# Kernel tuning notes

Measured on AMD Instinct MI355X. Metric: run time of the kernel, lower is better.

Reference implementation:

```python
import jax, jax.numpy as jnp
import numpy as np

L, HID, H, D = 2, 128, 8, 16  # layers, hidden, heads, head_dim
N, E = 50000, 800000
CLAMP = 5.0
BN_SCALE = 1.0 / np.sqrt(1.0 + 1e-5)  # eval BN with running mean 0, var 1


def signed_sqrt(s):
    # sqrt(relu(s)) - sqrt(relu(-s)), with safe gradients at 0
    pos = jnp.sqrt(jnp.where(s > 0, s, 1.0))
    neg = jnp.sqrt(jnp.where(s < 0, -s, 1.0))
    return jnp.where(s > 0, pos, 0.0) - jnp.where(s < 0, neg, 0.0)


def setup_inputs() -> dict:
    key = jax.random.key(0)
    ks = jax.random.split(key, 32)
    sc = 0.05
    inp = {
        "x": jax.random.normal(ks[0], (N, HID), jnp.float32),
        "edge_index": jax.random.randint(ks[1], (2, E), 0, N, jnp.int64)
        if jax.config.jax_enable_x64 else jax.random.randint(ks[1], (2, E), 0, N, jnp.int32),
        "edge_attr": jax.random.normal(ks[2], (E, HID), jnp.float32),
        "Wq": jax.random.normal(ks[3], (L, HID, HID), jnp.float32) * sc,
        "bq": jnp.zeros((L, HID), jnp.float32),
        "Wk": jax.random.normal(ks[4], (L, HID, HID), jnp.float32) * sc,
        "Wv": jax.random.normal(ks[5], (L, HID, HID), jnp.float32) * sc,
        "We": jax.random.normal(ks[6], (L, HID, 2 * HID), jnp.float32) * sc,
        "be": jnp.zeros((L, 2 * HID), jnp.float32),
        "Aw": jax.random.normal(ks[7], (L, D, H, 1), jnp.float32) * 0.2,
        "VeRow": jax.random.normal(ks[8], (L, D, H, D), jnp.float32) * sc,
        "Woh": jax.random.normal(ks[9], (L, HID, HID), jnp.float32) * sc,
        "boh": jnp.zeros((L, HID), jnp.float32),
        "Woe": jax.random.normal(ks[10], (L, HID, HID), jnp.float32) * sc,
        "boe": jnp.zeros((L, HID), jnp.float32),
        "deg_coef": jax.random.normal(ks[11], (L, 1, HID, 2), jnp.float32) * 0.2,
        "W1": jax.random.normal(ks[12], (L, HID, 2 * HID), jnp.float32) * sc,
        "b1": jnp.zeros((L, 2 * HID), jnp.float32),
        "W2": jax.random.normal(ks[13], (L, 2 * HID, HID), jnp.float32) * sc,
        "b2": jnp.zeros((L, HID), jnp.float32),
    }
    return inp


def _forward(x, edge_attr, edge_index, Wq, bq, Wk, Wv, We, be, Aw, VeRow,
             Woh, boh, Woe, boe, deg_coef, W1, b1, W2, b2):
    src, dst = edge_index[0], edge_index[1]
    n = x.shape[0]
    deg = jax.ops.segment_sum(jnp.ones_like(dst, jnp.float32), dst, num_segments=n)
    log_deg = jnp.log(deg + 1.0)[:, None]  # [N,1]

    for l in range(L):
        Qh = (x @ Wq[l] + bq[l]).reshape(n, H, D)
        Kh = (x @ Wk[l]).reshape(n, H, D)
        Vh = (x @ Wv[l]).reshape(n, H, D)
        Ep = (edge_attr @ We[l] + be[l]).reshape(-1, H, 2 * D)
        E_w, E_b = Ep[:, :, :D], Ep[:, :, D:]

        s = (Kh[src] + Qh[dst]) * E_w           # [E,H,D]
        s = signed_sqrt(s) + E_b
        e_t = jax.nn.relu(s)                     # [E,H,D]
        wE = e_t.reshape(-1, H * D)

        sc = jnp.einsum('ehd,dhc->ehc', e_t, Aw[l])   # [E,H,1]
        sc = jnp.clip(sc, -CLAMP, CLAMP)
        m = jax.ops.segment_max(sc, dst, num_segments=n)
        a = jnp.exp(sc - m[dst])
        denom = jax.ops.segment_sum(a, dst, num_segments=n)[dst] + 1e-16
        attn = a / denom                          # [E,H,1]

        wV = jax.ops.segment_sum(Vh[src] * attn, dst, num_segments=n)   # [N,H,D]
        rowV = jax.ops.segment_sum(e_t * attn, dst, num_segments=n)     # [N,H,D]
        wV = wV + jnp.einsum('nhd,dhc->nhc', rowV, VeRow[l])

        h = wV.reshape(n, H * D)
        h = h * deg_coef[l, :, :, 0] + (h * log_deg) * deg_coef[l, :, :, 1]
        h = h @ Woh[l] + boh[l]
        e = wE @ Woe[l] + boe[l]
        h = (x + h) * BN_SCALE
        e = (edge_attr + e) * BN_SCALE
        h2 = jax.nn.relu(h @ W1[l] + b1[l]) @ W2[l] + b2[l]
        h = (h + h2) * BN_SCALE
        x, edge_attr = h, e
    return x, edge_attr


def reference(x, edge_index, edge_attr, Wq, bq, Wk, Wv, We, be, Aw, VeRow,
              Woh, boh, Woe, boe, deg_coef, W1, b1, W2, b2):
    return _forward(x, edge_attr, edge_index, Wq, bq, Wk, Wv, We, be, Aw, VeRow,
                    Woh, boh, Woe, boe, deg_coef, W1, b1, W2, b2)
```

## Files before the change

kernel.cpp:

```cpp
#include <hip/hip_runtime.h>

#define NN 50000
#define NE 800000
#define CLAMPV 5.0f
#define BNS 0.9999950000374997f
#define EPKS 132
#define NBLK 49

typedef __attribute__((ext_vector_type(8))) short s16x8;
typedef __attribute__((ext_vector_type(8))) __bf16 bf16x8;
typedef __attribute__((ext_vector_type(4))) float f32x4;

__device__ inline f32x4 mfma16(s16x8 a, s16x8 b, f32x4 c) {
    return __builtin_amdgcn_mfma_f32_16x16x32_bf16(
        __builtin_bit_cast(bf16x8, a), __builtin_bit_cast(bf16x8, b), c, 0, 0, 0);
}

__device__ inline unsigned short bf16r(float f) {
    return __builtin_bit_cast(unsigned short, (__bf16)f);
}

__device__ inline int pk2(float a, float b) {
    return (int)(unsigned)bf16r(a) | ((int)(unsigned)bf16r(b) << 16);
}

__device__ inline float b2f(unsigned short u) {
    return __builtin_bit_cast(float, (unsigned)u << 16);
}


__global__ __launch_bounds__(256) void k_deg(const int* __restrict__ ei, int* __restrict__ deg) {
    int e = blockIdx.x * 256 + threadIdx.x;
    if (e < NE) atomicAdd(&deg[ei[NE + e]], 1);
}

__global__ __launch_bounds__(1024) void k_scan1(const int* __restrict__ deg, int* __restrict__ offs,
                                                int* __restrict__ bsum, float* __restrict__ logdeg) {
    __shared__ int sm[1024];
    int i = blockIdx.x * 1024 + threadIdx.x;
    int v = (i < NN) ? deg[i] : 0;
    if (i < NN) logdeg[i] = logf((float)v + 1.0f);
    sm[threadIdx.x] = v;
    __syncthreads();
    for (int s = 1; s < 1024; s <<= 1) {
        int t = (threadIdx.x >= s) ? sm[threadIdx.x - s] : 0;
        __syncthreads();
        sm[threadIdx.x] += t;
        __syncthreads();
    }
    if (i < NN) offs[i + 1] = sm[threadIdx.x];
    if (threadIdx.x == 1023) bsum[blockIdx.x] = sm[1023];
    if (blockIdx.x == 0 && threadIdx.x == 0) offs[0] = 0;
}

__global__ __launch_bounds__(1024) void k_scan3(int* __restrict__ offs, const int* __restrict__ bsum) {
    __shared__ int pre;
    if (threadIdx.x == 0) {
        int acc = 0;
        for (int i = 0; i < (int)blockIdx.x; ++i) acc += bsum[i];
        pre = acc;
    }
    __syncthreads();
    int i = blockIdx.x * 1024 + threadIdx.x;
    if (i < NN) offs[i + 1] += pre;
}

__global__ __launch_bounds__(256) void k_fill(const int* __restrict__ ei, const int* __restrict__ offs,
                                              int* __restrict__ cursor, int* __restrict__ csr_src,
                                              int* __restrict__ epos) {
    int e = blockIdx.x * 256 + threadIdx.x;
    if (e < NE) {
        int d = ei[NE + e];
        int pos = offs[d] + atomicAdd(&cursor[d], 1);
        csr_src[pos] = ei[e];
        epos[e] = pos;
    }
}

#define PL_A (128*256)
#define PL_B (128*128)
__global__ __launch_bounds__(256) void k_packAll(
    const float* __restrict__ We,  const float* __restrict__ Woe, const float* __restrict__ Wq,
    const float* __restrict__ Wk,  const float* __restrict__ Wv,  const float* __restrict__ Woh,
    const float* __restrict__ W1,  const float* __restrict__ W2,  const float* __restrict__ VR,
    short* __restrict__ Wep,  short* __restrict__ Woep, short* __restrict__ Wqp,
    short* __restrict__ Wkp,  short* __restrict__ Wvp,  short* __restrict__ Wohp,
    short* __restrict__ W1p,  short* __restrict__ W2p,  short* __restrict__ VRp) {
    int s = blockIdx.x * 256 + threadIdx.x;
    const float* W; short* out; int ncol, perL; bool vr = false;
    if (s < 2 * PL_A) { W = We; out = Wep; ncol = 256; perL = PL_A; }
    else if ((s -= 2 * PL_A) < 2 * PL_B) { W = Woe; out = Woep; ncol = 128; perL = PL_B; }
    else if ((s -= 2 * PL_B) < 2 * PL_B) { W = Wq;  out = Wqp;  ncol = 128; perL = PL_B; }
    else if ((s -= 2 * PL_B) < 2 * PL_B) { W = Wk;  out = Wkp;  ncol = 128; perL = PL_B; }
    else if ((s -= 2 * PL_B) < 2 * PL_B) { W = Wv;  out = Wvp;  ncol = 128; perL = PL_B; }
    else if ((s -= 2 * PL_B) < 2 * PL_B) { W = Woh; out = Wohp; ncol = 128; perL = PL_B; }
    else if ((s -= 2 * PL_B) < 2 * PL_A) { W = W1;  out = W1p;  ncol = 256; perL = PL_A; }
    else if ((s -= 2 * PL_A) < 2 * PL_A) { W = W2;  out = W2p;  ncol = 128; perL = PL_A; }
    else if ((s -= 2 * PL_A) < 2 * PL_B) { W = VR;  out = VRp;  ncol = 128; perL = PL_B; vr = true; }
    else return;
    int l = s / perL, q = s % perL;
    int j = q & 7; int t2 = q >> 3; int kg = t2 & 3; t2 >>= 2;
    int col = t2 % ncol; int kt = t2 / ncol;
    int k = kt * 32 + kg * 8 + j;
    float v;
    if (vr) v = ((k >> 4) == (col >> 4)) ? VR[l * 2048 + (k & 15) * 128 + col] : 0.f;
    else    v = W[(size_t)l * perL + k * ncol + col];
    out[(size_t)l * perL + q] = (short)bf16r(v);
}


__global__ __launch_bounds__(512) void k_qkv(const float* __restrict__ x,
                                             const short* __restrict__ Wqp, const float* __restrict__ bq,
                                             const short* __restrict__ Wkp, const short* __restrict__ Wvp,
                                             unsigned short* __restrict__ Qh, unsigned short* __restrict__ Kh,
                                             unsigned short* __restrict__ Vh) {
    __shared__ short xsw[64 * 128];
    int t = threadIdx.x;
    int ci = t & 15, r0 = t >> 4;
    int n0 = blockIdx.x * 64;
    for (int rr = r0; rr < 64; rr += 32) {
        int n = n0 + rr;
        int4 pkv = make_int4(0, 0, 0, 0);
        if (n < NN) {
            const float4* src = (const float4*)(x + (size_t)n * 128 + ci * 8);
            float4 v0 = src[0], v1 = src[1];
            pkv.x = pk2(v0.x, v0.y); pkv.y = pk2(v0.z, v0.w);
            pkv.z = pk2(v1.x, v1.y); pkv.w = pk2(v1.z, v1.w);
        }
        int byte = (rr * 256 + ci * 16) ^ ((rr & 7) << 4);
        *(int4*)((char*)xsw + byte) = pkv;
    }
    __syncthreads();
    int lane = t & 63, w = t >> 6;
    int l15 = lane & 15, kg = lane >> 4;
    f32x4 acc[4][3];
#pragma unroll
    for (int m = 0; m < 4; ++m)
#pragma unroll
        for (int q = 0; q < 3; ++q) { acc[m][q][0] = 0.f; acc[m][q][1] = 0.f; acc[m][q][2] = 0.f; acc[m][q][3] = 0.f; }
    int col = w * 16 + l15;
#pragma unroll
    for (int kt = 0; kt < 4; ++kt) {
        s16x8 a[4];
#pragma unroll
        for (int m = 0; m < 4; ++m) {
            int row = m * 16 + l15;
            int abyte = (row * 256 + kt * 64 + kg * 16) ^ ((l15 & 7) << 4);
            a[m] = *(const s16x8*)((const char*)xsw + abyte);
        }
        size_t bo = ((size_t)((kt * 128 + col) * 4 + kg)) * 8;
        s16x8 bqf = *(const s16x8*)(Wqp + bo);
        s16x8 bkf = *(const s16x8*)(Wkp + bo);
        s16x8 bvf = *(const s16x8*)(Wvp + bo);
#pragma unroll
        for (int m = 0; m < 4; ++m) {
            acc[m][0] = mfma16(a[m], bqf, acc[m][0]);
            acc[m][1] = mfma16(a[m], bkf, acc[m][1]);
            acc[m][2] = mfma16(a[m], bvf, acc[m][2]);
        }
    }
    float bqv = bq[col];
#pragma unroll
    for (int m = 0; m < 4; ++m)
#pragma unroll
        for (int i = 0; i < 4; ++i) {
            int n = n0 + m * 16 + kg * 4 + i;
            if (n < NN) {
                Qh[(size_t)n * 128 + col] = bf16r(acc[m][0][i] + bqv);
                Kh[(size_t)n * 128 + col] = bf16r(acc[m][1][i]);
                Vh[(size_t)n * 128 + col] = bf16r(acc[m][2][i]);
            }
        }
}

template<bool IN_F32>
__global__ __launch_bounds__(512) void k_edgeA(const void* __restrict__ ea_, const int* __restrict__ ei,
                                               const int* __restrict__ epos,
                                               const short* __restrict__ Wep, const float* __restrict__ be,
                                               const float* __restrict__ Aw,
                                               const unsigned short* __restrict__ Qh,
                                               const unsigned short* __restrict__ Kh,
                                               unsigned char* __restrict__ e8, float* __restrict__ sc,
                                               const short* __restrict__ Woep, const float* __restrict__ boe,
                                               void* __restrict__ eout_) {
    __shared__ short eas[64 * 128];
    __shared__ int epts[64 * EPKS];
    const float* eaf = (const float*)ea_;
    const unsigned short* eab = (const unsigned short*)ea_;
    unsigned short* eout_b = (unsigned short*)eout_;
    float* eout_f = (float*)eout_;

    int e0 = blockIdx.x * 64;
    int t = threadIdx.x;
    int ci = t & 15, r0 = t >> 4;
    int eA = e0 + r0, eB = eA + 32;
    int siA = ei[eA], diA = ei[NE + eA], posA = epos[eA];
    int siB = ei[eB], diB = ei[NE + eB], posB = epos[eB];

    {
#pragma unroll
        for (int h = 0; h < 2; ++h) {
            int rr = r0 + h * 32;
            int4 pkv;
            if (IN_F32) {
                const float4* src = (const float4*)(eaf + (size_t)(e0 + rr) * 128 + ci * 8);
                float4 v0 = src[0], v1 = src[1];
                pkv.x = pk2(v0.x, v0.y); pkv.y = pk2(v0.z, v0.w);
                pkv.z = pk2(v1.x, v1.y); pkv.w = pk2(v1.z, v1.w);
            } else {
                pkv = *(const int4*)(eab + (size_t)(e0 + rr) * 128 + ci * 8);
            }
            int byte = (rr * 256 + ci * 16) ^ ((rr & 7) << 4);
            *(int4*)((char*)eas + byte) = pkv;
        }
    }
    __syncthreads();
    union { int4 v; unsigned short us[8]; } kuA, quA, kuB, quB;
    kuA.v = *(const int4*)(Kh + (size_t)siA * 128 + ci * 8);
    quA.v = *(const int4*)(Qh + (size_t)diA * 128 + ci * 8);
    kuB.v = *(const int4*)(Kh + (size_t)siB * 128 + ci * 8);
    quB.v = *(const int4*)(Qh + (size_t)diB * 128 + ci * 8);

    int lane = t & 63, w = t >> 6;
    int l15 = lane & 15, kg = lane >> 4;
    {
        f32x4 acc[4][2];
#pragma unroll
        for (int m = 0; m < 4; ++m)
#pragma unroll
            for (int q = 0; q < 2; ++q) { acc[m][q][0] = 0.f; acc[m][q][1] = 0.f; acc[m][q][2] = 0.f; acc[m][q][3] = 0.f; }
#pragma unroll
        for (int kt = 0; kt < 4; ++kt) {
            s16x8 a[4];
#pragma unroll
            for (int m = 0; m < 4; ++m) {
                int row = m * 16 + l15;
                int abyte = (row * 256 + kt * 64 + kg * 16) ^ ((l15 & 7) << 4);
                a[m] = *(const s16x8*)((const char*)eas + abyte);
            }
#pragma unroll
            for (int q = 0; q < 2; ++q) {
                int col = w * 32 + q * 16 + l15;
                s16x8 b = *(const s16x8*)(Wep + ((size_t)((kt * 256 + col) * 4 + kg)) * 8);
#pragma unroll
                for (int m = 0; m < 4; ++m) acc[m][q] = mfma16(a[m], b, acc[m][q]);
            }
        }
        float bw = be[w * 32 + l15], bb = be[w * 32 + 16 + l15];
#pragma unroll
        for (int m = 0; m < 4; ++m)
#pragma unroll
            for (int i = 0; i < 4; ++i) {
                int row = m * 16 + kg * 4 + i;
                epts[row * EPKS + w * 16 + l15] = pk2(acc[m][0][i] + bw, acc[m][1][i] + bb);
            }
    }
    __syncthreads();
    int4 wA0, wA1, wB0, wB1;
    {
        const int4* pA = (const int4*)(epts + r0 * EPKS + ci * 8);
        wA0 = pA[0]; wA1 = pA[1];
        const int4* pB = (const int4*)(epts + (r0 + 32) * EPKS + ci * 8);
        wB0 = pB[0]; wB1 = pB[1];
    }
    __syncthreads();
    {
        int hh = ci >> 1, dbase = (ci & 1) * 8;
        float aw[8];
#pragma unroll
        for (int j = 0; j < 8; ++j) aw[j] = Aw[(dbase + j) * 8 + hh];
#pragma unroll
        for (int h = 0; h < 2; ++h) {
            int r = r0 + h * 32;
            int pos = h ? posB : posA;
            const unsigned short* kus = h ? kuB.us : kuA.us;
            const unsigned short* qus = h ? quB.us : quA.us;
            const int4 w0 = h ? wB0 : wA0;
            const int4 w1 = h ? wB1 : wA1;
            int prs[8] = {w0.x, w0.y, w0.z, w0.w, w1.x, w1.y, w1.z, w1.w};
            float p = 0.f;
            float etv[8];
#pragma unroll
            for (int j = 0; j < 8; ++j) {
                int pr = prs[j];
                float ew = b2f((unsigned short)pr);
                float ebv = b2f((unsigned short)((unsigned)pr >> 16));
                float kq = b2f(kus[j]) + b2f(qus[j]);
                float sv = kq * ew;
                float ss = copysignf(sqrtf(fabsf(sv)), sv);
                float et = fmaxf(ss + ebv, 0.f);
                etv[j] = et;
                p += et * aw[j];
            }
            int lo = __builtin_amdgcn_cvt_pk_fp8_f32(etv[0], etv[1], 0, 0);
            lo = __builtin_amdgcn_cvt_pk_fp8_f32(etv[2], etv[3], lo, 1);
            int hi = __builtin_amdgcn_cvt_pk_fp8_f32(etv[4], etv[5], 0, 0);
            hi = __builtin_amdgcn_cvt_pk_fp8_f32(etv[6], etv[7], hi, 1);
            *(int2*)(e8 + (size_t)pos * 128 + ci * 8) = make_int2(lo, hi);
            int4 pkv;
            pkv.x = pk2(etv[0], etv[1]); pkv.y = pk2(etv[2], etv[3]);
            pkv.z = pk2(etv[4], etv[5]); pkv.w = pk2(etv[6], etv[7]);
            int byte = (r * 256 + ci * 16) ^ ((r & 7) << 4);
            *(int4*)((char*)epts + byte) = pkv;
            p += __shfl_xor(p, 1);
            if ((ci & 1) == 0) {
                float s = fminf(fmaxf(p, -CLAMPV), CLAMPV);
                sc[(size_t)pos * 8 + hh] = s;
            }
        }
    }
    __syncthreads();
    {
        f32x4 acc[4];
#pragma unroll
        for (int m = 0; m < 4; ++m) { acc[m][0] = 0.f; acc[m][1] = 0.f; acc[m][2] = 0.f; acc[m][3] = 0.f; }
        int col = w * 16 + l15;
#pragma unroll
        for (int kt = 0; kt < 4; ++kt) {
            s16x8 a[4];
#pragma unroll
            for (int m = 0; m < 4; ++m) {
                int row = m * 16 + l15;
                int abyte = (row * 256 + kt * 64 + kg * 16) ^ ((l15 & 7) << 4);
                a[m] = *(const s16x8*)((const char*)epts + abyte);
            }
            s16x8 b = *(const s16x8*)(Woep + ((size_t)((kt * 128 + col) * 4 + kg)) * 8);
#pragma unroll
            for (int m = 0; m < 4; ++m) acc[m] = mfma16(a[m], b, acc[m]);
        }
        float bb = boe[col];
#pragma unroll
        for (int m = 0; m < 4; ++m)
#pragma unroll
            for (int i = 0; i < 4; ++i) {
                int rr = m * 16 + kg * 4 + i;
                int rbyte = (rr * 256 + col * 2) ^ ((rr & 7) << 4);
                float res = b2f(*(const unsigned short*)((const char*)eas + rbyte));
                size_t idx = (size_t)(e0 + rr) * 128 + col;
                float v = (res + acc[m][i] + bb) * BNS;
                if (IN_F32) eout_b[idx] = bf16r(v);
                else        eout_f[idx] = v;
            }
    }
}

__global__ __launch_bounds__(64) void k_nattn(const int* __restrict__ offs, const int* __restrict__ csr_src,
                                              const float* __restrict__ sc,
                                              const unsigned char* __restrict__ e8,
                                              const unsigned short* __restrict__ Vh,
                                              unsigned short* __restrict__ wVb,
                                              unsigned short* __restrict__ rowVb) {
    int n = blockIdx.x;
    int lane = threadIdx.x;
    int beg = offs[n], end = offs[n + 1];
    int h = lane & 7, es = lane >> 3;
    float m = -1e30f;
    for (int i = beg + es; i < end; i += 8)
        m = fmaxf(m, sc[(size_t)i * 8 + h]);
#pragma unroll
    for (int off = 8; off < 64; off <<= 1) m = fmaxf(m, __shfl_xor(m, off));
    int hv = lane >> 3;
    float mv = __shfl(m, hv);
    float dsum = 0.f, av0 = 0.f, av1 = 0.f, ar0 = 0.f, ar1 = 0.f;
    for (int i = beg; i < end; ++i) {
        float a = expf(sc[(size_t)i * 8 + hv] - mv);
        dsum += a;
        int s = csr_src[i];
        int v = ((const int*)Vh)[(size_t)s * 64 + lane];
        int u8 = ((const unsigned short*)e8)[(size_t)i * 64 + lane];
        av0 += b2f((unsigned short)v) * a;
        av1 += b2f((unsigned short)((unsigned)v >> 16)) * a;
        ar0 += __builtin_amdgcn_cvt_f32_fp8(u8, 0) * a;
        ar1 += __builtin_amdgcn_cvt_f32_fp8(u8, 1) * a;
    }
    float inv = 1.f / (dsum + 1e-16f);
    ((int*)wVb)[(size_t)n * 64 + lane]   = pk2(av0 * inv, av1 * inv);
    ((int*)rowVb)[(size_t)n * 64 + lane] = pk2(ar0 * inv, ar1 * inv);
}

template<bool EMIT>
__global__ __launch_bounds__(256) void k_nodeB(
    const unsigned short* __restrict__ wVb, const unsigned short* __restrict__ rowVb,
    const short* __restrict__ VRp, const float* __restrict__ dc,
    const float* __restrict__ logdeg, const float* __restrict__ x,
    const short* __restrict__ Wohp, const float* __restrict__ boh,
    const short* __restrict__ W1p, const float* __restrict__ b1,
    const short* __restrict__ W2p, const float* __restrict__ b2,
    float* __restrict__ xout,
    const short* __restrict__ Wqp2, const float* __restrict__ bq2,
    const short* __restrict__ Wkp2, const short* __restrict__ Wvp2,
    unsigned short* __restrict__ Qh2, unsigned short* __restrict__ Kh2,
    unsigned short* __restrict__ Vh2) {
    __shared__ short bufA[32 * 128];
    __shared__ short bufU[32 * 256];
    int n0 = blockIdx.x * 32;
    int t = threadIdx.x;
    int ci = t & 15, r0 = t >> 4;
    {
#pragma unroll
        for (int h = 0; h < 2; ++h) {
            int rr = r0 + h * 16, n = n0 + rr;
            int4 pkv = make_int4(0, 0, 0, 0);
            if (n < NN) pkv = *(const int4*)(rowVb + (size_t)n * 128 + ci * 8);
            int byte = (rr * 256 + ci * 16) ^ ((rr & 7) << 4);
            *(int4*)((char*)bufA + byte) = pkv;
        }
    }
    __syncthreads();
    int lane = t & 63, w = t >> 6;
    int l15 = lane & 15, kg = lane >> 4;
    int cq[2] = {w * 32 + l15, w * 32 + 16 + l15};
    {
        f32x4 acc[2][2];
#pragma unroll
        for (int m = 0; m < 2; ++m)
#pragma unroll
            for (int q = 0; q < 2; ++q)
#pragma unroll
                for (int i = 0; i < 4; ++i) {
                    int n = n0 + m * 16 + kg * 4 + i;
                    acc[m][q][i] = (n < NN) ? b2f(wVb[(size_t)n * 128 + cq[q]]) : 0.f;
                }
#pragma unroll
        for (int kt = 0; kt < 4; ++kt) {
            s16x8 a[2];
#pragma unroll
            for (int m = 0; m < 2; ++m) {
                int row = m * 16 + l15;
                int abyte = (row * 256 + kt * 64 + kg * 16) ^ ((l15 & 7) << 4);
                a[m] = *(const s16x8*)((const char*)bufA + abyte);
            }
#pragma unroll
            for (int q = 0; q < 2; ++q) {
                s16x8 b = *(const s16x8*)(VRp + ((size_t)((kt * 128 + cq[q]) * 4 + kg)) * 8);
#pragma unroll
                for (int m = 0; m < 2; ++m) acc[m][q] = mfma16(a[m], b, acc[m][q]);
            }
        }
#pragma unroll
        for (int q = 0; q < 2; ++q) {
            float d0 = dc[cq[q] * 2], d1 = dc[cq[q] * 2 + 1];
#pragma unroll
            for (int m = 0; m < 2; ++m)
#pragma unroll
                for (int i = 0; i < 4; ++i) {
                    int rr = m * 16 + kg * 4 + i, n = n0 + rr;
                    float ld = (n < NN) ? logdeg[n] : 0.f;
                    float hs = acc[m][q][i] * (d0 + ld * d1);
                    int byte = (rr * 256 + cq[q] * 2) ^ ((rr & 7) << 4);
                    *(unsigned short*)((char*)bufU + byte) = bf16r(hs);
                }
        }
    }
    __syncthreads();
    float h1r[2][2][4];
    {
        f32x4 acc[2][2];
#pragma unroll
        for (int m = 0; m < 2; ++m)
#pragma unroll
            for (int q = 0; q < 2; ++q) { acc[m][q][0] = 0.f; acc[m][q][1] = 0.f; acc[m][q][2] = 0.f; acc[m][q][3] = 0.f; }
#pragma unroll
        for (int kt = 0; kt < 4; ++kt) {
            s16x8 a[2];
#pragma unroll
            for (int m = 0; m < 2; ++m) {
                int row = m * 16 + l15;
                int abyte = (row * 256 + kt * 64 + kg * 16) ^ ((l15 & 7) << 4);
                a[m] = *(const s16x8*)((const char*)bufU + abyte);
            }
#pragma unroll
            for (int q = 0; q < 2; ++q) {
                s16x8 b = *(const s16x8*)(Wohp + ((size_t)((kt * 128 + cq[q]) * 4 + kg)) * 8);
#pragma unroll
                for (int m = 0; m < 2; ++m) acc[m][q] = mfma16(a[m], b, acc[m][q]);
            }
        }
#pragma unroll
        for (int q = 0; q < 2; ++q) {
            float bb = boh[cq[q]];
#pragma unroll
            for (int m = 0; m < 2; ++m)
#pragma unroll
                for (int i = 0; i < 4; ++i) {
                    int rr = m * 16 + kg * 4 + i, n = n0 + rr;
                    float xv = (n < NN) ? x[(size_t)n * 128 + cq[q]] : 0.f;
                    float h1 = (xv + acc[m][q][i] + bb) * BNS;
                    h1r[m][q][i] = h1;
                    int byte = (rr * 256 + cq[q] * 2) ^ ((rr & 7) << 4);
                    *(unsigned short*)((char*)bufA + byte) = bf16r(h1);
                }
        }
    }
    __syncthreads();
    {
        f32x4 acc[2][4];
#pragma unroll
        for (int m = 0; m < 2; ++m)
#pragma unroll
            for (int q = 0; q < 4; ++q) { acc[m][q][0] = 0.f; acc[m][q][1] = 0.f; acc[m][q][2] = 0.f; acc[m][q][3] = 0.f; }
#pragma unroll
        for (int kt = 0; kt < 4; ++kt) {
            s16x8 a[2];
#pragma unroll
            for (int m = 0; m < 2; ++m) {
                int row = m * 16 + l15;
                int abyte = (row * 256 + kt * 64 + kg * 16) ^ ((l15 & 7) << 4);
                a[m] = *(const s16x8*)((const char*)bufA + abyte);
            }
#pragma unroll
            for (int q = 0; q < 4; ++q) {
                int colq = w * 64 + q * 16 + l15;
                s16x8 b = *(const s16x8*)(W1p + ((size_t)((kt * 256 + colq) * 4 + kg)) * 8);
#pragma unroll
                for (int m = 0; m < 2; ++m) acc[m][q] = mfma16(a[m], b, acc[m][q]);
            }
        }
        __syncthreads();
#pragma unroll
        for (int q = 0; q < 4; ++q) {
            int colq = w * 64 + q * 16 + l15;
            float bb = b1[colq];
#pragma unroll
            for (int m = 0; m < 2; ++m)
#pragma unroll
                for (int i = 0; i < 4; ++i) {
                    int rr = m * 16 + kg * 4 + i;
                    float us = fmaxf(acc[m][q][i] + bb, 0.f);
                    int byte = (rr * 512 + colq * 2) ^ ((rr & 7) << 4);
                    *(unsigned short*)((char*)bufU + byte) = bf16r(us);
                }
        }
    }
    __syncthreads();
    {
        f32x4 acc[2][2];
#pragma unroll
        for (int m = 0; m < 2; ++m)
#pragma unroll
            for (int q = 0; q < 2; ++q) { acc[m][q][0] = 0.f; acc[m][q][1] = 0.f; acc[m][q][2] = 0.f; acc[m][q][3] = 0.f; }
#pragma unroll
        for (int kt = 0; kt < 8; ++kt) {
            s16x8 a[2];
#pragma unroll
            for (int m = 0; m < 2; ++m) {
                int row = m * 16 + l15;
                int abyte = (row * 512 + kt * 64 + kg * 16) ^ ((l15 & 7) << 4);
                a[m] = *(const s16x8*)((const char*)bufU + abyte);
            }
#pragma unroll
            for (int q = 0; q < 2; ++q) {
                s16x8 b = *(const s16x8*)(W2p + ((size_t)((kt * 128 + cq[q]) * 4 + kg)) * 8);
#pragma unroll
                for (int m = 0; m < 2; ++m) acc[m][q] = mfma16(a[m], b, acc[m][q]);
            }
        }
#pragma unroll
        for (int q = 0; q < 2; ++q) {
            float bb = b2[cq[q]];
#pragma unroll
            for (int m = 0; m < 2; ++m)
#pragma unroll
                for (int i = 0; i < 4; ++i) {
                    int rr = m * 16 + kg * 4 + i, n = n0 + rr;
                    float outv = (h1r[m][q][i] + acc[m][q][i] + bb) * BNS;
                    if (n < NN) xout[(size_t)n * 128 + cq[q]] = outv;
                    if (EMIT) {
                        int byte = (rr * 256 + cq[q] * 2) ^ ((rr & 7) << 4);
                        *(unsigned short*)((char*)bufA + byte) = bf16r(outv);
                    }
                }
        }
    }
    if (EMIT) {
        __syncthreads();
        f32x4 acc[2][2][3];
#pragma unroll
        for (int m = 0; m < 2; ++m)
#pragma unroll
            for (int q = 0; q < 2; ++q)
#pragma unroll
                for (int o = 0; o < 3; ++o) { acc[m][q][o][0] = 0.f; acc[m][q][o][1] = 0.f; acc[m][q][o][2] = 0.f; acc[m][q][o][3] = 0.f; }
#pragma unroll
        for (int kt = 0; kt < 4; ++kt) {
            s16x8 a[2];
#pragma unroll
            for (int m = 0; m < 2; ++m) {
                int row = m * 16 + l15;
                int abyte = (row * 256 + kt * 64 + kg * 16) ^ ((l15 & 7) << 4);
                a[m] = *(const s16x8*)((const char*)bufA + abyte);
            }
#pragma unroll
            for (int q = 0; q < 2; ++q) {
                size_t bo = ((size_t)((kt * 128 + cq[q]) * 4 + kg)) * 8;
                s16x8 bqf = *(const s16x8*)(Wqp2 + bo);
                s16x8 bkf = *(const s16x8*)(Wkp2 + bo);
                s16x8 bvf = *(const s16x8*)(Wvp2 + bo);
#pragma unroll
                for (int m = 0; m < 2; ++m) {
                    acc[m][q][0] = mfma16(a[m], bqf, acc[m][q][0]);
                    acc[m][q][1] = mfma16(a[m], bkf, acc[m][q][1]);
                    acc[m][q][2] = mfma16(a[m], bvf, acc[m][q][2]);
                }
            }
        }
#pragma unroll
        for (int q = 0; q < 2; ++q) {
            float bqv = bq2[cq[q]];
#pragma unroll
            for (int m = 0; m < 2; ++m)
#pragma unroll
                for (int i = 0; i < 4; ++i) {
                    int n = n0 + m * 16 + kg * 4 + i;
                    if (n < NN) {
                        Qh2[(size_t)n * 128 + cq[q]] = bf16r(acc[m][q][0][i] + bqv);
                        Kh2[(size_t)n * 128 + cq[q]] = bf16r(acc[m][q][1][i]);
                        Vh2[(size_t)n * 128 + cq[q]] = bf16r(acc[m][q][2][i]);
                    }
                }
        }
    }
}


extern "C" void kernel_launch(void* const* d_in, const int* in_sizes, int n_in,
                              void* d_out, int out_size, void* d_ws, size_t ws_size,
                              hipStream_t stream) {
    (void)in_sizes; (void)n_in; (void)out_size; (void)ws_size;
    const float* x_in0  = (const float*)d_in[0];
    const int*   ei     = (const int*)d_in[1];
    const float* ea_in0 = (const float*)d_in[2];
    const float* Wq = (const float*)d_in[3];
    const float* bq = (const float*)d_in[4];
    const float* Wk = (const float*)d_in[5];
    const float* Wv = (const float*)d_in[6];
    const float* We = (const float*)d_in[7];
    const float* be = (const float*)d_in[8];
    const float* Aw = (const float*)d_in[9];
    const float* VeRow = (const float*)d_in[10];
    const float* Woh = (const float*)d_in[11];
    const float* boh = (const float*)d_in[12];
    const float* Woe = (const float*)d_in[13];
    const float* boe = (const float*)d_in[14];
    const float* dc  = (const float*)d_in[15];
    const float* W1 = (const float*)d_in[16];
    const float* b1 = (const float*)d_in[17];
    const float* W2 = (const float*)d_in[18];
    const float* b2 = (const float*)d_in[19];

    char* ws = (char*)d_ws;
    size_t off = 0;
    auto alloc = [&](size_t bytes) { void* p = ws + off; off = (off + bytes + 255) & ~(size_t)255; return p; };
    int*   deg    = (int*)alloc((size_t)NN * 4);
    int*   cursor = (int*)alloc((size_t)NN * 4);
    int*   offs   = (int*)alloc((size_t)(NN + 1) * 4);
    int*   bsum   = (int*)alloc((size_t)64 * 4);
    int*   csr_src= (int*)alloc((size_t)NE * 4);
    int*   epos   = (int*)alloc((size_t)NE * 4);
    float* logdeg = (float*)alloc((size_t)NN * 4);
    unsigned short* Qh  = (unsigned short*)alloc((size_t)NN * 128 * 2);
    unsigned short* Kh  = (unsigned short*)alloc((size_t)NN * 128 * 2);
    unsigned short* Vh  = (unsigned short*)alloc((size_t)NN * 128 * 2);
    unsigned short* Qh2 = (unsigned short*)alloc((size_t)NN * 128 * 2);
    unsigned short* Kh2 = (unsigned short*)alloc((size_t)NN * 128 * 2);
    unsigned short* Vh2 = (unsigned short*)alloc((size_t)NN * 128 * 2);
    unsigned char* e8   = (unsigned char*)alloc((size_t)NE * 128);
    unsigned short* ea_bf = (unsigned short*)alloc((size_t)NE * 128 * 2);
    float* sc     = (float*)alloc((size_t)NE * 8 * 4);
    unsigned short* wVb   = (unsigned short*)alloc((size_t)NN * 128 * 2);
    unsigned short* rowVb = (unsigned short*)alloc((size_t)NN * 128 * 2);
    short* Wep    = (short*)alloc((size_t)2 * 128 * 256 * 2);
    short* Woep   = (short*)alloc((size_t)2 * 128 * 128 * 2);
    short* Wqp    = (short*)alloc((size_t)2 * 128 * 128 * 2);
    short* Wkp    = (short*)alloc((size_t)2 * 128 * 128 * 2);
    short* Wvp    = (short*)alloc((size_t)2 * 128 * 128 * 2);
    short* Wohp   = (short*)alloc((size_t)2 * 128 * 128 * 2);
    short* W1p    = (short*)alloc((size_t)2 * 128 * 256 * 2);
    short* W2p    = (short*)alloc((size_t)2 * 256 * 128 * 2);
    short* VRp    = (short*)alloc((size_t)2 * 128 * 128 * 2);

    float* out_x = (float*)d_out;
    float* out_e = out_x + (size_t)NN * 128;

    hipError_t err;
    err = hipMemsetAsync(deg, 0, (size_t)NN * 4, stream); (void)err;
    err = hipMemsetAsync(cursor, 0, (size_t)NN * 4, stream); (void)err;

    k_deg<<<(NE + 255) / 256, 256, 0, stream>>>(ei, deg);
    k_scan1<<<NBLK, 1024, 0, stream>>>(deg, offs, bsum, logdeg);
    k_scan3<<<NBLK, 1024, 0, stream>>>(offs, bsum);
    k_fill<<<(NE + 255) / 256, 256, 0, stream>>>(ei, offs, cursor, csr_src, epos);
    k_packAll<<<1536, 256, 0, stream>>>(We, Woe, Wq, Wk, Wv, Woh, W1, W2, VeRow,
                                        Wep, Woep, Wqp, Wkp, Wvp, Wohp, W1p, W2p, VRp);

    k_qkv<<<(NN + 63) / 64, 512, 0, stream>>>(x_in0, Wqp, bq, Wkp, Wvp, Qh, Kh, Vh);
    k_edgeA<true><<<NE / 64, 512, 0, stream>>>(ea_in0, ei, epos, Wep, be, Aw, Qh, Kh,
                                               e8, sc, Woep, boe, ea_bf);
    k_nattn<<<NN, 64, 0, stream>>>(offs, csr_src, sc, e8, Vh, wVb, rowVb);
    k_nodeB<true><<<(NN + 31) / 32, 256, 0, stream>>>(
        wVb, rowVb, VRp, dc, logdeg, x_in0,
        Wohp, boh, W1p, b1, W2p, b2, out_x,
        Wqp + 128 * 128, bq + 128, Wkp + 128 * 128, Wvp + 128 * 128, Qh2, Kh2, Vh2);

    k_edgeA<false><<<NE / 64, 512, 0, stream>>>(ea_bf, ei, epos, Wep + 128 * 256, be + 256,
                                                Aw + 128, Qh2, Kh2, e8, sc,
                                                Woep + 128 * 128, boe + 128, out_e);
    k_nattn<<<NN, 64, 0, stream>>>(offs, csr_src, sc, e8, Vh2, wVb, rowVb);
    k_nodeB<false><<<(NN + 31) / 32, 256, 0, stream>>>(
        wVb, rowVb, VRp + 128 * 128, dc + 256, logdeg, out_x,
        Wohp + 128 * 128, boh + 128, W1p + 128 * 256, b1 + 256, W2p + 256 * 128, b2 + 128, out_x,
        nullptr, nullptr, nullptr, nullptr, nullptr, nullptr, nullptr);
}
```

Measured before the change: 967.1 us.

## Store edge projections as fp8 in LDS and drop softmax max pass

The edge projection (weight, bias pairs) is now packed to fp8 in shared memory instead of bf16 pairs, which halves LDS footprint and the per-thread read width in the edge kernel. The node attention kernel drops the segment-max pass, relying on scores being clamped to [-5,5] so exp cannot overflow, uses fast __expf, and unrolls the edge loop by two. These changes reduce LDS traffic and remove a full read pass over scores, at the cost of lower precision in the edge projection values.

```diff
diff --git a/kernel.cpp b/kernel.cpp
--- a/kernel.cpp
+++ b/kernel.cpp
@@ -4,7 +4,7 @@
 #define NE 800000
 #define CLAMPV 5.0f
 #define BNS 0.9999950000374997f
-#define EPKS 132
+#define EPS 136
 #define NBLK 49
 
 typedef __attribute__((ext_vector_type(8))) short s16x8;
@@ -184,7 +184,7 @@
                                                const short* __restrict__ Woep, const float* __restrict__ boe,
                                                void* __restrict__ eout_) {
     __shared__ short eas[64 * 128];
-    __shared__ int epts[64 * EPKS];
+    __shared__ short epts[64 * EPS];
     const float* eaf = (const float*)ea_;
     const unsigned short* eab = (const unsigned short*)ea_;
     unsigned short* eout_b = (unsigned short*)eout_;
@@ -252,16 +252,15 @@
 #pragma unroll
             for (int i = 0; i < 4; ++i) {
                 int row = m * 16 + kg * 4 + i;
-                epts[row * EPKS + w * 16 + l15] = pk2(acc[m][0][i] + bw, acc[m][1][i] + bb);
-            }
-    }
-    __syncthreads();
-    int4 wA0, wA1, wB0, wB1;
-    {
-        const int4* pA = (const int4*)(epts + r0 * EPKS + ci * 8);
-        wA0 = pA[0]; wA1 = pA[1];
-        const int4* pB = (const int4*)(epts + (r0 + 32) * EPKS + ci * 8);
-        wB0 = pB[0]; wB1 = pB[1];
+                int p8 = __builtin_amdgcn_cvt_pk_fp8_f32(acc[m][0][i] + bw, acc[m][1][i] + bb, 0, 0);
+                epts[row * EPS + w * 16 + l15] = (short)p8;
+            }
+    }
+    __syncthreads();
+    int4 wA, wB;
+    {
+        wA = *(const int4*)(epts + (size_t)r0 * EPS + ci * 8);
+        wB = *(const int4*)(epts + (size_t)(r0 + 32) * EPS + ci * 8);
     }
     __syncthreads();
     {
@@ -275,22 +274,23 @@
             int pos = h ? posB : posA;
             const unsigned short* kus = h ? kuB.us : kuA.us;
             const unsigned short* qus = h ? quB.us : quA.us;
-            const int4 w0 = h ? wB0 : wA0;
-            const int4 w1 = h ? wB1 : wA1;
-            int prs[8] = {w0.x, w0.y, w0.z, w0.w, w1.x, w1.y, w1.z, w1.w};
+            const int4 ww = h ? wB : wA;
+            int words[4] = {ww.x, ww.y, ww.z, ww.w};
             float p = 0.f;
             float etv[8];
 #pragma unroll
-            for (int j = 0; j < 8; ++j) {
-                int pr = prs[j];
-                float ew = b2f((unsigned short)pr);
-                float ebv = b2f((unsigned short)((unsigned)pr >> 16));
-                float kq = b2f(kus[j]) + b2f(qus[j]);
-                float sv = kq * ew;
-                float ss = copysignf(sqrtf(fabsf(sv)), sv);
-                float et = fmaxf(ss + ebv, 0.f);
-                etv[j] = et;
-                p += et * aw[j];
+            for (int k = 0; k < 4; ++k) {
+                float ew0 = __builtin_amdgcn_cvt_f32_fp8(words[k], 0);
+                float eb0 = __builtin_amdgcn_cvt_f32_fp8(words[k], 1);
+                float ew1 = __builtin_amdgcn_cvt_f32_fp8(words[k], 2);
+                float eb1 = __builtin_amdgcn_cvt_f32_fp8(words[k], 3);
+                float kq0 = b2f(kus[2 * k]) + b2f(qus[2 * k]);
+                float kq1 = b2f(kus[2 * k + 1]) + b2f(qus[2 * k + 1]);
+                float sv0 = kq0 * ew0, sv1 = kq1 * ew1;
+                float et0 = fmaxf(copysignf(sqrtf(fabsf(sv0)), sv0) + eb0, 0.f);
+                float et1 = fmaxf(copysignf(sqrtf(fabsf(sv1)), sv1) + eb1, 0.f);
+                etv[2 * k] = et0; etv[2 * k + 1] = et1;
+                p += et0 * aw[2 * k] + et1 * aw[2 * k + 1];
             }
             int lo = __builtin_amdgcn_cvt_pk_fp8_f32(etv[0], etv[1], 0, 0);
             lo = __builtin_amdgcn_cvt_pk_fp8_f32(etv[2], etv[3], lo, 1);
@@ -353,17 +353,10 @@
     int n = blockIdx.x;
     int lane = threadIdx.x;
     int beg = offs[n], end = offs[n + 1];
-    int h = lane & 7, es = lane >> 3;
-    float m = -1e30f;
-    for (int i = beg + es; i < end; i += 8)
-        m = fmaxf(m, sc[(size_t)i * 8 + h]);
-#pragma unroll
-    for (int off = 8; off < 64; off <<= 1) m = fmaxf(m, __shfl_xor(m, off));
     int hv = lane >> 3;
-    float mv = __shfl(m, hv);
     float dsum = 0.f, av0 = 0.f, av1 = 0.f, ar0 = 0.f, ar1 = 0.f;
-    for (int i = beg; i < end; ++i) {
-        float a = expf(sc[(size_t)i * 8 + hv] - mv);
+    auto body = [&](int i) {
+        float a = __expf(sc[(size_t)i * 8 + hv]);
         dsum += a;
         int s = csr_src[i];
         int v = ((const int*)Vh)[(size_t)s * 64 + lane];
@@ -372,7 +365,10 @@
         av1 += b2f((unsigned short)((unsigned)v >> 16)) * a;
         ar0 += __builtin_amdgcn_cvt_f32_fp8(u8, 0) * a;
         ar1 += __builtin_amdgcn_cvt_f32_fp8(u8, 1) * a;
-    }
+    };
+    int i = beg;
+    for (; i + 2 <= end; i += 2) { body(i); body(i + 1); }
+    for (; i < end; ++i) body(i);
     float inv = 1.f / (dsum + 1e-16f);
     ((int*)wVb)[(size_t)n * 64 + lane]   = pk2(av0 * inv, av1 * inv);
     ((int*)rowVb)[(size_t)n * 64 + lane] = pk2(ar0 * inv, ar1 * inv);
```

Result: faster. 905.1 us (-6.4%).
